# Kernel optimization log

Hardware: AMD Instinct MI355X
Metric: run time of the kernel (lower is better)

Reference implementation:

```python
import jax, jax.numpy as jnp
import numpy as np

N, E, F_NODE, F_EDGE, H, C = 25000, 50000, 7, 2, 4, 512
HC = H * C  # 2048


def setup_inputs() -> dict:
    key = jax.random.key(0)
    ks = jax.random.split(key, 20)
    p = lambda k, shp: (jax.random.normal(k, shp, dtype=jnp.float32) * 0.02)
    return {
        "x": jax.random.normal(ks[0], (N, F_NODE), dtype=jnp.float32),
        "edge_attr": jax.random.normal(ks[1], (E, F_EDGE), dtype=jnp.float32),
        "edge_index": jax.random.randint(ks[2], (2, E), 0, N, dtype=jnp.int64),
        "W_node": p(ks[3], (F_NODE, C)), "b_node": jnp.zeros((C,), jnp.float32),
        "W_edge": p(ks[4], (F_EDGE, C)), "b_edge": jnp.zeros((C,), jnp.float32),
        "W_l": p(ks[5], (C, HC)), "b_l": jnp.zeros((HC,), jnp.float32),
        "W_r": p(ks[6], (C, HC)), "b_r": jnp.zeros((HC,), jnp.float32),
        "W_le": p(ks[7], (C, HC)),  # lin_edge has no bias in PyG GATv2Conv
        "att": p(ks[8], (H, C)),
        "conv_bias": jnp.zeros((HC,), jnp.float32),
        "W_d1": p(ks[9], (HC, C)), "b_d1": jnp.zeros((C,), jnp.float32),
        "W_d2": p(ks[10], (C, 6)), "b_d2": jnp.zeros((6,), jnp.float32),
    }


def reference(x, edge_attr, edge_index, W_node, b_node, W_edge, b_edge,
              W_l, b_l, W_r, b_r, W_le, att, conv_bias, W_d1, b_d1, W_d2, b_d2):
    n = x.shape[0]
    src, dst = edge_index[0], edge_index[1]
    # encoders
    h = jax.nn.relu(x @ W_node + b_node)                  # [N, C]
    ea = jax.nn.relu(edge_attr @ W_edge + b_edge)         # [E, C]
    # GATv2Conv (heads=4, concat, edge_dim, add_self_loops=False)
    xl = (h @ W_l + b_l).reshape(n, H, C)                 # source transform
    xr = (h @ W_r + b_r).reshape(n, H, C)                 # target transform
    ee = (ea @ W_le).reshape(-1, H, C)                    # [E, H, C]
    m = xl[src] + xr[dst] + ee                            # [E, H, C]
    s = jax.nn.leaky_relu(m, negative_slope=0.2)
    logits = jnp.einsum('ehc,hc->eh', s, att)             # [E, H]
    # segment softmax over destination nodes
    mx = jax.ops.segment_max(logits, dst, num_segments=n)
    ex = jnp.exp(logits - mx[dst])
    den = jax.ops.segment_sum(ex, dst, num_segments=n)
    alpha = ex / (den[dst] + 1e-16)                       # [E, H]
    out = jax.ops.segment_sum(alpha[..., None] * xl[src], dst, num_segments=n)
    out = out.reshape(n, HC) + conv_bias                  # [N, 2048]
    # decoder + sigmoid (mode != 'train')
    pred = jax.nn.relu(out @ W_d1 + b_d1) @ W_d2 + b_d2   # [N, 6]
    return jax.nn.sigmoid(pred)
```

## Files before the change

### kernel.cpp

```cpp
#include <hip/hip_runtime.h>
#include <hip/hip_bf16.h>

typedef __attribute__((ext_vector_type(8))) short short8;
typedef __attribute__((ext_vector_type(4))) float f32x4;
typedef unsigned int uint32;

#define GLD16(g, l) __builtin_amdgcn_global_load_lds( \
    (const __attribute__((address_space(1))) unsigned int*)(g), \
    (__attribute__((address_space(3))) unsigned int*)(l), 16, 0, 0)

__device__ __forceinline__ float bfu(unsigned short u) {
    union { uint32 v; float f; } x; x.v = ((uint32)u) << 16; return x.f;
}
__device__ __forceinline__ void storev(float* p, float v) { *p = v; }
__device__ __forceinline__ void storev(__hip_bfloat16* p, float v) { *p = __float2bfloat16(v); }

__global__ __launch_bounds__(256) void transpose_bf16(
    const float* __restrict__ W, __hip_bfloat16* __restrict__ WT, int K, int N)
{
    __shared__ float tile[32][33];
    int k0 = blockIdx.x * 32, n0 = blockIdx.y * 32;
    int tx = threadIdx.x & 31, ty = threadIdx.x >> 5;
    #pragma unroll
    for (int i = 0; i < 32; i += 8)
        tile[ty + i][tx] = W[(size_t)(k0 + ty + i) * N + n0 + tx];
    __syncthreads();
    #pragma unroll
    for (int i = 0; i < 32; i += 8)
        WT[(size_t)(n0 + ty + i) * K + k0 + tx] = __float2bfloat16(tile[tx][ty + i]);
}

__global__ __launch_bounds__(256) void cast_bf16(
    const float* __restrict__ W, __hip_bfloat16* __restrict__ O, int total)
{
    int idx = blockIdx.x * 256 + threadIdx.x;
    if (idx < total) O[idx] = __float2bfloat16(W[idx]);
}

__global__ __launch_bounds__(256) void encode_nodes(
    const float* __restrict__ x, const float* __restrict__ Wn,
    const float* __restrict__ bn, __hip_bfloat16* __restrict__ h, int Nn)
{
    int idx = blockIdx.x * 256 + threadIdx.x;
    if (idx >= Nn * 512) return;
    int n = idx >> 9, c = idx & 511;
    float acc = bn[c];
    #pragma unroll
    for (int f = 0; f < 7; ++f) acc += x[n * 7 + f] * Wn[f * 512 + c];
    h[idx] = __float2bfloat16(fmaxf(acc, 0.f));
}

__global__ __launch_bounds__(256) void encode_edges_sorted(
    const float* __restrict__ eat, const int* __restrict__ elist,
    const float* __restrict__ We, const float* __restrict__ be,
    __hip_bfloat16* __restrict__ ea, int E)
{
    int idx = blockIdx.x * 256 + threadIdx.x;
    if (idx >= E * 512) return;
    int p = idx >> 9, c = idx & 511;
    int e = elist[p];
    float v = fmaf(eat[e * 2], We[c], fmaf(eat[e * 2 + 1], We[512 + c], be[c]));
    ea[idx] = __float2bfloat16(fmaxf(v, 0.f));
}

template <typename OutT, bool HAS_BIAS>
__global__ __launch_bounds__(256) void mfma_gemm(
    const __hip_bfloat16* __restrict__ A, int lda, long az,
    const __hip_bfloat16* __restrict__ BT, int ldb, long bz,
    const float* __restrict__ bias, long biasz,
    OutT* __restrict__ C, int ldc, long cz, int M, int K)
{
    __shared__ uint4 As4[1024];
    __shared__ uint4 Bs4[1024];
    A  += (long)blockIdx.z * az;
    BT += (long)blockIdx.z * bz;
    C  += (long)blockIdx.z * cz;
    if (HAS_BIAS) bias += (long)blockIdx.z * biasz;
    const int t = threadIdx.x, lane = t & 63, w = t >> 6;
    const int wr = (w >> 1) * 64, wc = (w & 1) * 64;
    const int col0 = blockIdx.x * 128, row0 = blockIdx.y * 128;
    const int lr = lane & 15, lg = lane >> 4;
    const int srow8 = lane >> 3;
    const int sch   = (lane & 7) ^ srow8;
    const int rx = lr & 7;

    const __hip_bfloat16* ApL = A + (size_t)(row0 + srow8) * lda + sch * 8;
    const __hip_bfloat16* BpL = BT + (size_t)(col0 + srow8) * ldb + sch * 8;

    f32x4 acc[4][4];
    #pragma unroll
    for (int m = 0; m < 4; ++m)
        #pragma unroll
        for (int n = 0; n < 4; ++n) acc[m][n] = 0.f;

    for (int k0 = 0; k0 < K; k0 += 64) {
        #pragma unroll
        for (int j = 0; j < 4; ++j) {
            int rb = (w + 4 * j) * 8;
            GLD16(ApL + (size_t)rb * lda + k0, As4 + (w + 4 * j) * 64);
            GLD16(BpL + (size_t)rb * ldb + k0, Bs4 + (w + 4 * j) * 64);
        }
        __syncthreads();
        #pragma unroll
        for (int kk = 0; kk < 2; ++kk) {
            short8 af[4], bfrag[4];
            #pragma unroll
            for (int m = 0; m < 4; ++m) {
                int row = wr + m * 16 + lr;
                af[m] = *(const short8*)((const char*)As4 + row * 128 + (((kk * 4 + lg) ^ rx) << 4));
            }
            #pragma unroll
            for (int n = 0; n < 4; ++n) {
                int row = wc + n * 16 + lr;
                bfrag[n] = *(const short8*)((const char*)Bs4 + row * 128 + (((kk * 4 + lg) ^ rx) << 4));
            }
            #pragma unroll
            for (int m = 0; m < 4; ++m)
                #pragma unroll
                for (int n = 0; n < 4; ++n)
                    acc[m][n] = __builtin_amdgcn_mfma_f32_16x16x32_bf16(af[m], bfrag[n], acc[m][n], 0, 0, 0);
        }
        __syncthreads();
    }

    #pragma unroll
    for (int m = 0; m < 4; ++m) {
        #pragma unroll
        for (int r = 0; r < 4; ++r) {
            int gr = row0 + wr + m * 16 + lg * 4 + r;
            if (gr >= M) continue;
            #pragma unroll
            for (int n = 0; n < 4; ++n) {
                int gc = col0 + wc + n * 16 + lr;
                float v = acc[m][n][r];
                if (HAS_BIAS) v += bias[gc];
                storev(&C[(size_t)gr * ldc + gc], v);
            }
        }
    }
}

__global__ __launch_bounds__(256) void edge_mfma_logits(
    const __hip_bfloat16* __restrict__ ea,
    const __hip_bfloat16* __restrict__ WleT,
    const __hip_bfloat16* __restrict__ XL,
    const __hip_bfloat16* __restrict__ XR,
    const int* __restrict__ ssrc,
    const int* __restrict__ sdst,
    const float* __restrict__ att,
    float* __restrict__ logits,
    int E)
{
    __shared__ uint4 As4[1024];
    __shared__ uint4 Bs4[1024];
    __shared__ int srcs[128], dsts[128];
    const int t = threadIdx.x, lane = t & 63, w = t >> 6;
    const int wr = (w >> 1) * 64, wc = (w & 1) * 64;
    const int col0 = blockIdx.x * 128, row0 = blockIdx.y * 128;
    const int lr = lane & 15, lg = lane >> 4;
    const int srow8 = lane >> 3;
    const int sch   = (lane & 7) ^ srow8;
    const int rx = lr & 7;

    if (t < 128) {
        int ge = row0 + t;
        bool ok = ge < E;
        srcs[t] = ok ? ssrc[ge] : 0;
        dsts[t] = ok ? sdst[ge] : 0;
    }
    const __hip_bfloat16* ApL = ea + (size_t)(row0 + srow8) * 512 + sch * 8;
    const __hip_bfloat16* BpL = WleT + (size_t)(col0 + srow8) * 512 + sch * 8;
    __syncthreads();

    f32x4 acc[4][4];
    #pragma unroll
    for (int m = 0; m < 4; ++m)
        #pragma unroll
        for (int n = 0; n < 4; ++n) acc[m][n] = 0.f;

    for (int k0 = 0; k0 < 512; k0 += 64) {
        #pragma unroll
        for (int j = 0; j < 4; ++j) {
            int rb = (w + 4 * j) * 8;
            GLD16(ApL + (size_t)rb * 512 + k0, As4 + (w + 4 * j) * 64);
            GLD16(BpL + (size_t)rb * 512 + k0, Bs4 + (w + 4 * j) * 64);
        }
        __syncthreads();
        #pragma unroll
        for (int kk = 0; kk < 2; ++kk) {
            short8 af[4], bfrag[4];
            #pragma unroll
            for (int m = 0; m < 4; ++m) {
                int row = wr + m * 16 + lr;
                af[m] = *(const short8*)((const char*)As4 + row * 128 + (((kk * 4 + lg) ^ rx) << 4));
            }
            #pragma unroll
            for (int n = 0; n < 4; ++n) {
                int row = wc + n * 16 + lr;
                bfrag[n] = *(const short8*)((const char*)Bs4 + row * 128 + (((kk * 4 + lg) ^ rx) << 4));
            }
            #pragma unroll
            for (int m = 0; m < 4; ++m)
                #pragma unroll
                for (int n = 0; n < 4; ++n)
                    acc[m][n] = __builtin_amdgcn_mfma_f32_16x16x32_bf16(af[m], bfrag[n], acc[m][n], 0, 0, 0);
        }
        __syncthreads();
    }

    const int hh = col0 >> 9;
    float attv[4];
    #pragma unroll
    for (int n = 0; n < 4; ++n)
        attv[n] = att[hh * 512 + ((col0 + wc + n * 16 + lr) & 511)];
    float part[4][4];
    #pragma unroll
    for (int m = 0; m < 4; ++m)
        #pragma unroll
        for (int r = 0; r < 4; ++r) part[m][r] = 0.f;

    const int prt = (lane & 3) * 8;
    const int r0e = w * 16 + (lane >> 2);
    const int s0 = srcs[r0e], s1 = srcs[r0e + 64];
    const int d0 = dsts[r0e], d1 = dsts[r0e + 64];

    #pragma unroll
    for (int pair = 0; pair < 2; ++pair) {
        #pragma unroll
        for (int sp = 0; sp < 2; ++sp) {
            int ch = pair + sp * 2;
            int cc = col0 + ch * 32;
            GLD16(XL + (size_t)s0 * 2048 + cc + prt, As4 + sp * 512 + w * 64);
            GLD16(XL + (size_t)s1 * 2048 + cc + prt, As4 + sp * 512 + (w + 4) * 64);
            GLD16(XR + (size_t)d0 * 2048 + cc + prt, Bs4 + sp * 512 + w * 64);
            GLD16(XR + (size_t)d1 * 2048 + cc + prt, Bs4 + sp * 512 + (w + 4) * 64);
        }
        __syncthreads();
        #pragma unroll
        for (int sp = 0; sp < 2; ++sp) {
            int ch = pair + sp * 2;
            const char* AsB = (const char*)(As4 + sp * 512);
            const char* BsB = (const char*)(Bs4 + sp * 512);
            #pragma unroll
            for (int n = 0; n < 4; ++n) {
                if (((wc + n * 16) >> 5) != ch) continue;
                int colin = ((n & 1) << 4) + lr;
                #pragma unroll
                for (int m = 0; m < 4; ++m) {
                    #pragma unroll
                    for (int r = 0; r < 4; ++r) {
                        int row = wr + m * 16 + lg * 4 + r;
                        float xl = bfu(*(const unsigned short*)(AsB + row * 64 + colin * 2));
                        float xr = bfu(*(const unsigned short*)(BsB + row * 64 + colin * 2));
                        float mv = acc[m][n][r] + xl + xr;
                        part[m][r] += attv[n] * ((mv > 0.f) ? mv : 0.2f * mv);
                    }
                }
            }
        }
        __syncthreads();
    }
    #pragma unroll
    for (int m = 0; m < 4; ++m) {
        #pragma unroll
        for (int r = 0; r < 4; ++r) {
            float p = part[m][r];
            p += __shfl_xor(p, 1); p += __shfl_xor(p, 2);
            p += __shfl_xor(p, 4); p += __shfl_xor(p, 8);
            int ge = row0 + wr + m * 16 + lg * 4 + r;
            if (lr == 0 && ge < E) atomicAdd(&logits[ge * 4 + hh], p);
        }
    }
}

__global__ __launch_bounds__(256) void count_dst(
    const int* __restrict__ ei, int* __restrict__ cnt, int E)
{
    int e = blockIdx.x * 256 + threadIdx.x;
    if (e < E) atomicAdd(&cnt[ei[E + e]], 1);
}

__global__ __launch_bounds__(1024) void scan_kernel(
    const int* __restrict__ cnt, int* __restrict__ offs, int N)
{
    __shared__ int wsum[16];
    __shared__ int stot;
    __shared__ int carry_s;
    int t = threadIdx.x, lane = t & 63, w = t >> 6;
    if (t == 0) carry_s = 0;
    __syncthreads();
    for (int base = 0; base < N; base += 1024) {
        int v = (base + t < N) ? cnt[base + t] : 0;
        int x = v;
        #pragma unroll
        for (int off = 1; off < 64; off <<= 1) {
            int y = __shfl_up(x, off);
            if (lane >= off) x += y;
        }
        if (lane == 63) wsum[w] = x;
        __syncthreads();
        if (w == 0 && lane < 16) {
            int v0 = wsum[lane];
            int s = v0;
            #pragma unroll
            for (int off = 1; off < 16; off <<= 1) {
                int y = __shfl_up(s, off);
                if (lane >= off) s += y;
            }
            wsum[lane] = s - v0;
            if (lane == 15) stot = s;
        }
        __syncthreads();
        if (base + t < N) offs[base + t] = carry_s + wsum[w] + x - v;
        __syncthreads();
        if (t == 0) carry_s += stot;
    }
    __syncthreads();
    if (t == 0) offs[N] = carry_s;
}

__global__ __launch_bounds__(256) void fill_elist(
    const int* __restrict__ ei, const int* __restrict__ offs,
    int* __restrict__ cnt2, int* __restrict__ elist,
    int* __restrict__ ssrc, int* __restrict__ sdst, int E)
{
    int e = blockIdx.x * 256 + threadIdx.x;
    if (e >= E) return;
    int d = ei[E + e];
    int p = offs[d] + atomicAdd(&cnt2[d], 1);
    elist[p] = e;
    ssrc[p] = ei[e];
    sdst[p] = d;
}

__global__ __launch_bounds__(256) void bias_init(
    const float* __restrict__ bd1, float* __restrict__ bias2, float* __restrict__ blw)
{
    int j = blockIdx.x * 256 + threadIdx.x;
    if (j < 512) { bias2[j] = bd1[j]; blw[j] = 0.f; }
}
__global__ __launch_bounds__(256) void bias_acc(
    const float* __restrict__ cb, const float* __restrict__ bl,
    const float* __restrict__ Wd1, float* __restrict__ bias2, float* __restrict__ blw)
{
    int g = blockIdx.x * 256 + threadIdx.x;
    int j = g & 511, slice = g >> 9;
    float pa = 0.f, pb = 0.f;
    for (int k = slice * 128; k < slice * 128 + 128; ++k) {
        float wv = Wd1[(size_t)k * 512 + j];
        pa += cb[k] * wv;
        pb += bl[k] * wv;
    }
    atomicAdd(&bias2[j], pa);
    atomicAdd(&blw[j], pb);
}

__global__ __launch_bounds__(256) void gat_out(
    const __hip_bfloat16* __restrict__ Y,
    const int* __restrict__ ssrc, const int* __restrict__ offs,
    const float* __restrict__ logits,
    const float* __restrict__ bias2, const float* __restrict__ blw,
    const float* __restrict__ Wd2,
    const float* __restrict__ bd2,
    float* __restrict__ out, int N)
{
    __shared__ float wds[512 * 6];
    int t = threadIdx.x;
    for (int i = t; i < 512 * 6; i += 256) wds[i] = Wd2[i];
    __syncthreads();
    int w = t >> 6, lane = t & 63;
    int dst = blockIdx.x * 4 + w;
    if (dst >= N) return;
    int s = offs[dst], cntE = offs[dst + 1] - s;

    float den[4] = {0.f, 0.f, 0.f, 0.f};
    for (int i = 0; i < cntE; ++i) {
        #pragma unroll
        for (int h = 0; h < 4; ++h) den[h] += expf(logits[(s + i) * 4 + h]);
    }
    float acc[8] = {0.f, 0.f, 0.f, 0.f, 0.f, 0.f, 0.f, 0.f};
    for (int i = 0; i < cntE; ++i) {
        int p = s + i;
        int src = ssrc[p];
        #pragma unroll
        for (int h = 0; h < 4; ++h) {
            float al = expf(logits[p * 4 + h]) / (den[h] + 1e-16f);
            uint4 q = *(const uint4*)((const unsigned short*)Y
                        + ((size_t)src * 4 + h) * 512 + lane * 8);
            acc[0] += al * bfu((unsigned short)(q.x & 0xffff));
            acc[1] += al * bfu((unsigned short)(q.x >> 16));
            acc[2] += al * bfu((unsigned short)(q.y & 0xffff));
            acc[3] += al * bfu((unsigned short)(q.y >> 16));
            acc[4] += al * bfu((unsigned short)(q.z & 0xffff));
            acc[5] += al * bfu((unsigned short)(q.z >> 16));
            acc[6] += al * bfu((unsigned short)(q.w & 0xffff));
            acc[7] += al * bfu((unsigned short)(q.w >> 16));
        }
    }
    float gate = (cntE > 0) ? 1.f : 0.f;
    float p6[6] = {0.f, 0.f, 0.f, 0.f, 0.f, 0.f};
    #pragma unroll
    for (int j = 0; j < 8; ++j) {
        int c = lane * 8 + j;
        float u = fmaxf(acc[j] + bias2[c] + gate * blw[c], 0.f);
        #pragma unroll
        for (int jj = 0; jj < 6; ++jj) p6[jj] += u * wds[c * 6 + jj];
    }
    #pragma unroll
    for (int off = 32; off; off >>= 1)
        #pragma unroll
        for (int jj = 0; jj < 6; ++jj) p6[jj] += __shfl_down(p6[jj], off);
    if (lane == 0) {
        #pragma unroll
        for (int jj = 0; jj < 6; ++jj)
            out[(size_t)dst * 6 + jj] = 1.f / (1.f + expf(-(p6[jj] + bd2[jj])));
    }
}

extern "C" void kernel_launch(void* const* d_in, const int* in_sizes, int n_in,
                              void* d_out, int out_size, void* d_ws, size_t ws_size,
                              hipStream_t stream)
{
    const float* x         = (const float*)d_in[0];
    const float* edge_attr = (const float*)d_in[1];
    const int*   ei        = (const int*)d_in[2];
    const float* W_node = (const float*)d_in[3],  *b_node = (const float*)d_in[4];
    const float* W_edge = (const float*)d_in[5],  *b_edge = (const float*)d_in[6];
    const float* W_l    = (const float*)d_in[7],  *b_l    = (const float*)d_in[8];
    const float* W_r    = (const float*)d_in[9],  *b_r    = (const float*)d_in[10];
    const float* W_le   = (const float*)d_in[11];
    const float* att    = (const float*)d_in[12];
    const float* conv_bias = (const float*)d_in[13];
    const float* W_d1   = (const float*)d_in[14], *b_d1 = (const float*)d_in[15];
    const float* W_d2   = (const float*)d_in[16], *b_d2 = (const float*)d_in[17];
    float* out = (float*)d_out;

    const int N = in_sizes[0] / 7;
    const int E = in_sizes[1] / 2;
    const int MP = (N + 127) & ~127;
    const int EP = (E + 127) & ~127;

    char* ws = (char*)d_ws;
    const size_t szR0 = (size_t)EP * 512 * 2;
    const size_t szX  = (size_t)MP * 2048 * 2;
    const size_t szW  = (size_t)2048 * 512 * 2;
    const size_t szlg = (size_t)E * 4 * 4;
    const size_t szI  = (((size_t)(N + 1) * 4) + 15) & ~(size_t)15;
    const size_t o_XL = szR0;
    const size_t o_XR = o_XL + szX;
    const size_t o_W  = o_XR + szX;
    const size_t o_lg = o_W + 4 * szW;
    const size_t o_b2 = o_lg + szlg;
    const size_t o_blw = o_b2 + 2048;
    const size_t o_bc = o_blw + 2048;
    const size_t o_cnt = o_bc + 4096 * 4;
    const size_t o_cnt2 = o_cnt + szI;
    const size_t o_off = o_cnt2 + szI;
    const size_t o_el = o_off + szI;
    const size_t o_ss = o_el + (size_t)E * 4;
    const size_t o_sd = o_ss + (size_t)E * 4;
    const size_t need = o_sd + (size_t)E * 4;
    if (ws_size < need) return;

    __hip_bfloat16* h   = (__hip_bfloat16*)ws;
    __hip_bfloat16* ea  = (__hip_bfloat16*)ws;
    __hip_bfloat16* XL  = (__hip_bfloat16*)(ws + o_XL);
    __hip_bfloat16* XR  = (__hip_bfloat16*)(ws + o_XR);
    __hip_bfloat16* Y   = XR;
    __hip_bfloat16* WlT = (__hip_bfloat16*)(ws + o_W);
    __hip_bfloat16* WrT = WlT + szW / 2;
    __hip_bfloat16* WleT= WrT + szW / 2;
    __hip_bfloat16* WcombT = WleT + szW / 2;
    __hip_bfloat16* Wd1T_t = (__hip_bfloat16*)(ws + o_XL);
    __hip_bfloat16* Wlbf_t = (__hip_bfloat16*)(ws + o_XL + szW);
    float* logits = (float*)(ws + o_lg);
    float* bias2  = (float*)(ws + o_b2);
    float* blw    = (float*)(ws + o_blw);
    float* bcat   = (float*)(ws + o_bc);
    int* cnt   = (int*)(ws + o_cnt);
    int* cnt2  = (int*)(ws + o_cnt2);
    int* offs  = (int*)(ws + o_off);
    int* elist = (int*)(ws + o_el);
    int* ssrc  = (int*)(ws + o_ss);
    int* sdst  = (int*)(ws + o_sd);

    hipMemsetAsync(logits, 0, szlg, stream);
    hipMemsetAsync(cnt, 0, szI, stream);
    hipMemsetAsync(cnt2, 0, szI, stream);
    hipMemcpyAsync(bcat, b_l, 2048 * 4, hipMemcpyDeviceToDevice, stream);
    hipMemcpyAsync(bcat + 2048, b_r, 2048 * 4, hipMemcpyDeviceToDevice, stream);

    dim3 gT(512 / 32, 2048 / 32);
    transpose_bf16<<<gT, 256, 0, stream>>>(W_l,  WlT, 512, 2048);
    transpose_bf16<<<gT, 256, 0, stream>>>(W_r,  WrT, 512, 2048);
    transpose_bf16<<<gT, 256, 0, stream>>>(W_le, WleT, 512, 2048);
    dim3 gT2(2048 / 32, 512 / 32);
    transpose_bf16<<<gT2, 256, 0, stream>>>(W_d1, Wd1T_t, 2048, 512);
    cast_bf16<<<(512 * 2048 + 255) / 256, 256, 0, stream>>>(W_l, Wlbf_t, 512 * 2048);

    dim3 gWc(512 / 128, 512 / 128, 4);
    mfma_gemm<__hip_bfloat16, false><<<gWc, 256, 0, stream>>>(
        Wd1T_t, 2048, 512, Wlbf_t, 2048, 512, nullptr, 0,
        WcombT, 512, (long)512 * 512, 512, 512);

    bias_init<<<2, 256, 0, stream>>>(b_d1, bias2, blw);
    bias_acc<<<32, 256, 0, stream>>>(conv_bias, b_l, W_d1, bias2, blw);

    count_dst<<<(E + 255) / 256, 256, 0, stream>>>(ei, cnt, E);
    scan_kernel<<<1, 1024, 0, stream>>>(cnt, offs, N);
    fill_elist<<<(E + 255) / 256, 256, 0, stream>>>(ei, offs, cnt2, elist, ssrc, sdst, E);

    encode_nodes<<<(N * 512 + 255) / 256, 256, 0, stream>>>(x, W_node, b_node, h, N);

    const int MB = MP / 128;
    dim3 gNode(2048 / 128, MB, 2);
    mfma_gemm<__hip_bfloat16, true><<<gNode, 256, 0, stream>>>(
        h, 512, 0, WlT, 512, (long)2048 * 512, bcat, 2048,
        XL, 2048, (long)MP * 2048, N, 512);

    encode_edges_sorted<<<(E * 512 + 255) / 256, 256, 0, stream>>>(
        edge_attr, elist, W_edge, b_edge, ea, E);

    dim3 gE(16, EP / 128);
    edge_mfma_logits<<<gE, 256, 0, stream>>>(ea, WleT, XL, XR, ssrc, sdst, att, logits, E);

    encode_nodes<<<(N * 512 + 255) / 256, 256, 0, stream>>>(x, W_node, b_node, h, N);

    dim3 gY(2048 / 128, MB);
    mfma_gemm<__hip_bfloat16, false><<<gY, 256, 0, stream>>>(
        h, 512, 0, WcombT, 512, 0, nullptr, 0, Y, 2048, 0, N, 512);

    gat_out<<<(N + 3) / 4, 256, 0, stream>>>(Y, ssrc, offs, logits,
                                             bias2, blw, W_d2, b_d2, out, N);
}
```

Measured before the change: 710.9 us.

## Aggregate encoded node features before the combined projection GEMM

The order of neighbor aggregation and the fused W_l·W_d1 projection is swapped. Each edge now gathers a 512-wide bf16 node feature row and accumulates it per head into a 2048-wide buffer G. A new GEMM with K=2048 then maps G to the 512-wide decoder hidden layer, fusing the bias, the zero-in-degree gate and ReLU. A separate decoder kernel applies the final 6-output layer and sigmoid. This cuts random gather traffic per edge by four times, but adds full writes and reads of the G and Z intermediates and one more kernel launch.

```diff
diff --git a/kernel.cpp b/kernel.cpp
--- a/kernel.cpp
+++ b/kernel.cpp
@@ -135,6 +135,79 @@
                 float v = acc[m][n][r];
                 if (HAS_BIAS) v += bias[gc];
                 storev(&C[(size_t)gr * ldc + gc], v);
+            }
+        }
+    }
+}
+
+__global__ __launch_bounds__(256) void z_gemm(
+    const __hip_bfloat16* __restrict__ A,
+    const __hip_bfloat16* __restrict__ BT,
+    const float* __restrict__ bias2, const float* __restrict__ blw,
+    const int* __restrict__ offs,
+    float* __restrict__ C, int M)
+{
+    __shared__ uint4 As4[1024];
+    __shared__ uint4 Bs4[1024];
+    const int t = threadIdx.x, lane = t & 63, w = t >> 6;
+    const int wr = (w >> 1) * 64, wc = (w & 1) * 64;
+    const int col0 = blockIdx.x * 128, row0 = blockIdx.y * 128;
+    const int lr = lane & 15, lg = lane >> 4;
+    const int srow8 = lane >> 3;
+    const int sch   = (lane & 7) ^ srow8;
+    const int rx = lr & 7;
+
+    const __hip_bfloat16* ApL = A + (size_t)(row0 + srow8) * 2048 + sch * 8;
+    const __hip_bfloat16* BpL = BT + (size_t)(col0 + srow8) * 2048 + sch * 8;
+
+    f32x4 acc[4][4];
+    #pragma unroll
+    for (int m = 0; m < 4; ++m)
+        #pragma unroll
+        for (int n = 0; n < 4; ++n) acc[m][n] = 0.f;
+
+    for (int k0 = 0; k0 < 2048; k0 += 64) {
+        #pragma unroll
+        for (int j = 0; j < 4; ++j) {
+            int rb = (w + 4 * j) * 8;
+            GLD16(ApL + (size_t)rb * 2048 + k0, As4 + (w + 4 * j) * 64);
+            GLD16(BpL + (size_t)rb * 2048 + k0, Bs4 + (w + 4 * j) * 64);
+        }
+        __syncthreads();
+        #pragma unroll
+        for (int kk = 0; kk < 2; ++kk) {
+            short8 af[4], bfrag[4];
+            #pragma unroll
+            for (int m = 0; m < 4; ++m) {
+                int row = wr + m * 16 + lr;
+                af[m] = *(const short8*)((const char*)As4 + row * 128 + (((kk * 4 + lg) ^ rx) << 4));
+            }
+            #pragma unroll
+            for (int n = 0; n < 4; ++n) {
+                int row = wc + n * 16 + lr;
+                bfrag[n] = *(const short8*)((const char*)Bs4 + row * 128 + (((kk * 4 + lg) ^ rx) << 4));
+            }
+            #pragma unroll
+            for (int m = 0; m < 4; ++m)
+                #pragma unroll
+                for (int n = 0; n < 4; ++n)
+                    acc[m][n] = __builtin_amdgcn_mfma_f32_16x16x32_bf16(af[m], bfrag[n], acc[m][n], 0, 0, 0);
+        }
+        __syncthreads();
+    }
+
+    #pragma unroll
+    for (int m = 0; m < 4; ++m) {
+        #pragma unroll
+        for (int r = 0; r < 4; ++r) {
+            int gr = row0 + wr + m * 16 + lg * 4 + r;
+            if (gr >= M) continue;
+            float gate = (offs[gr + 1] > offs[gr]) ? 1.f : 0.f;
+            #pragma unroll
+            for (int n = 0; n < 4; ++n) {
+                int gc = col0 + wc + n * 16 + lr;
+                float v = acc[m][n][r] + bias2[gc] + gate * blw[gc];
+                C[(size_t)gr * 512 + gc] = fmaxf(v, 0.f);
             }
         }
     }
@@ -355,65 +428,78 @@
     atomicAdd(&blw[j], pb);
 }
 
-__global__ __launch_bounds__(256) void gat_out(
-    const __hip_bfloat16* __restrict__ Y,
+__global__ __launch_bounds__(256) void gat_agg(
+    const __hip_bfloat16* __restrict__ hfeat,
     const int* __restrict__ ssrc, const int* __restrict__ offs,
     const float* __restrict__ logits,
-    const float* __restrict__ bias2, const float* __restrict__ blw,
-    const float* __restrict__ Wd2,
-    const float* __restrict__ bd2,
-    float* __restrict__ out, int N)
+    __hip_bfloat16* __restrict__ G,
+    int N)
+{
+    int t = threadIdx.x;
+    int w = t >> 6, lane = t & 63;
+    int dst = blockIdx.x * 4 + w;
+    if (dst >= N) return;
+    int s = offs[dst], cntE = offs[dst + 1] - s;
+
+    float den[4] = {0.f, 0.f, 0.f, 0.f};
+    for (int i = 0; i < cntE; ++i) {
+        #pragma unroll
+        for (int hh = 0; hh < 4; ++hh) den[hh] += expf(logits[(s + i) * 4 + hh]);
+    }
+    float acc[4][8] = {};
+    for (int i = 0; i < cntE; ++i) {
+        int p = s + i;
+        int src = ssrc[p];
+        uint4 q = *(const uint4*)((const unsigned short*)hfeat + (size_t)src * 512 + lane * 8);
+        float hv[8];
+        hv[0] = bfu((unsigned short)(q.x & 0xffff)); hv[1] = bfu((unsigned short)(q.x >> 16));
+        hv[2] = bfu((unsigned short)(q.y & 0xffff)); hv[3] = bfu((unsigned short)(q.y >> 16));
+        hv[4] = bfu((unsigned short)(q.z & 0xffff)); hv[5] = bfu((unsigned short)(q.z >> 16));
+        hv[6] = bfu((unsigned short)(q.w & 0xffff)); hv[7] = bfu((unsigned short)(q.w >> 16));
+        #pragma unroll
+        for (int hh = 0; hh < 4; ++hh) {
+            float al = expf(logits[p * 4 + hh]) / (den[hh] + 1e-16f);
+            #pragma unroll
+            for (int j = 0; j < 8; ++j) acc[hh][j] += al * hv[j];
+        }
+    }
+    #pragma unroll
+    for (int hh = 0; hh < 4; ++hh) {
+        alignas(16) __hip_bfloat16 tmp[8];
+        #pragma unroll
+        for (int j = 0; j < 8; ++j) tmp[j] = __float2bfloat16(acc[hh][j]);
+        *(uint4*)((unsigned short*)G + ((size_t)dst * 4 + hh) * 512 + lane * 8) = *(const uint4*)tmp;
+    }
+}
+
+__global__ __launch_bounds__(256) void decoder(
+    const float* __restrict__ Z, const float* __restrict__ Wd2,
+    const float* __restrict__ bd2, float* __restrict__ out, int M)
 {
     __shared__ float wds[512 * 6];
     int t = threadIdx.x;
     for (int i = t; i < 512 * 6; i += 256) wds[i] = Wd2[i];
     __syncthreads();
-    int w = t >> 6, lane = t & 63;
-    int dst = blockIdx.x * 4 + w;
-    if (dst >= N) return;
-    int s = offs[dst], cntE = offs[dst + 1] - s;
-
-    float den[4] = {0.f, 0.f, 0.f, 0.f};
-    for (int i = 0; i < cntE; ++i) {
-        #pragma unroll
-        for (int h = 0; h < 4; ++h) den[h] += expf(logits[(s + i) * 4 + h]);
-    }
-    float acc[8] = {0.f, 0.f, 0.f, 0.f, 0.f, 0.f, 0.f, 0.f};
-    for (int i = 0; i < cntE; ++i) {
-        int p = s + i;
-        int src = ssrc[p];
-        #pragma unroll
-        for (int h = 0; h < 4; ++h) {
-            float al = expf(logits[p * 4 + h]) / (den[h] + 1e-16f);
-            uint4 q = *(const uint4*)((const unsigned short*)Y
-                        + ((size_t)src * 4 + h) * 512 + lane * 8);
-            acc[0] += al * bfu((unsigned short)(q.x & 0xffff));
-            acc[1] += al * bfu((unsigned short)(q.x >> 16));
-            acc[2] += al * bfu((unsigned short)(q.y & 0xffff));
-            acc[3] += al * bfu((unsigned short)(q.y >> 16));
-            acc[4] += al * bfu((unsigned short)(q.z & 0xffff));
-            acc[5] += al * bfu((unsigned short)(q.z >> 16));
-            acc[6] += al * bfu((unsigned short)(q.w & 0xffff));
-            acc[7] += al * bfu((unsigned short)(q.w >> 16));
-        }
-    }
-    float gate = (cntE > 0) ? 1.f : 0.f;
-    float p6[6] = {0.f, 0.f, 0.f, 0.f, 0.f, 0.f};
-    #pragma unroll
-    for (int j = 0; j < 8; ++j) {
-        int c = lane * 8 + j;
-        float u = fmaxf(acc[j] + bias2[c] + gate * blw[c], 0.f);
-        #pragma unroll
-        for (int jj = 0; jj < 6; ++jj) p6[jj] += u * wds[c * 6 + jj];
+    int node = (blockIdx.x * 256 + t) >> 6;
+    int lane = t & 63;
+    if (node >= M) return;
+    const float* zr = Z + (size_t)node * 512;
+    float p[6] = {0.f, 0.f, 0.f, 0.f, 0.f, 0.f};
+    #pragma unroll
+    for (int k = 0; k < 8; ++k) {
+        int c = lane + k * 64;
+        float a = zr[c];
+        #pragma unroll
+        for (int j = 0; j < 6; ++j) p[j] += a * wds[c * 6 + j];
     }
     #pragma unroll
     for (int off = 32; off; off >>= 1)
         #pragma unroll
-        for (int jj = 0; jj < 6; ++jj) p6[jj] += __shfl_down(p6[jj], off);
+        for (int j = 0; j < 6; ++j) p[j] += __shfl_down(p[j], off);
     if (lane == 0) {
         #pragma unroll
-        for (int jj = 0; jj < 6; ++jj)
-            out[(size_t)dst * 6 + jj] = 1.f / (1.f + expf(-(p6[jj] + bd2[jj])));
+        for (int j = 0; j < 6; ++j)
+            out[(size_t)node * 6 + j] = 1.f / (1.f + expf(-(p[j] + bd2[j])));
     }
 }
 
@@ -464,13 +550,14 @@
 
     __hip_bfloat16* h   = (__hip_bfloat16*)ws;
     __hip_bfloat16* ea  = (__hip_bfloat16*)ws;
+    float*          Z   = (float*)ws;
     __hip_bfloat16* XL  = (__hip_bfloat16*)(ws + o_XL);
     __hip_bfloat16* XR  = (__hip_bfloat16*)(ws + o_XR);
-    __hip_bfloat16* Y   = XR;
+    __hip_bfloat16* G   = XR;
     __hip_bfloat16* WlT = (__hip_bfloat16*)(ws + o_W);
     __hip_bfloat16* WrT = WlT + szW / 2;
     __hip_bfloat16* WleT= WrT + szW / 2;
-    __hip_bfloat16* WcombT = WleT + szW / 2;
+    __hip_bfloat16* WcombT2 = WleT + szW / 2;
     __hip_bfloat16* Wd1T_t = (__hip_bfloat16*)(ws + o_XL);
     __hip_bfloat16* Wlbf_t = (__hip_bfloat16*)(ws + o_XL + szW);
     float* logits = (float*)(ws + o_lg);
@@ -501,7 +588,7 @@
     dim3 gWc(512 / 128, 512 / 128, 4);
     mfma_gemm<__hip_bfloat16, false><<<gWc, 256, 0, stream>>>(
         Wd1T_t, 2048, 512, Wlbf_t, 2048, 512, nullptr, 0,
-        WcombT, 512, (long)512 * 512, 512, 512);
+        WcombT2, 2048, 512, 512, 512);
 
     bias_init<<<2, 256, 0, stream>>>(b_d1, bias2, blw);
     bias_acc<<<32, 256, 0, stream>>>(conv_bias, b_l, W_d1, bias2, blw);
@@ -525,11 +612,10 @@
     edge_mfma_logits<<<gE, 256, 0, stream>>>(ea, WleT, XL, XR, ssrc, sdst, att, logits, E);
 
     encode_nodes<<<(N * 512 + 255) / 256, 256, 0, stream>>>(x, W_node, b_node, h, N);
-
-    dim3 gY(2048 / 128, MB);
-    mfma_gemm<__hip_bfloat16, false><<<gY, 256, 0, stream>>>(
-        h, 512, 0, WcombT, 512, 0, nullptr, 0, Y, 2048, 0, N, 512);
-
-    gat_out<<<(N + 3) / 4, 256, 0, stream>>>(Y, ssrc, offs, logits,
-                                             bias2, blw, W_d2, b_d2, out, N);
-}
+    gat_agg<<<(N + 3) / 4, 256, 0, stream>>>(h, ssrc, offs, logits, G, N);
+
+    dim3 gZ(512 / 128, MB);
+    z_gemm<<<gZ, 256, 0, stream>>>(G, WcombT2, bias2, blw, offs, Z, N);
+
+    decoder<<<(N * 64 + 255) / 256, 256, 0, stream>>>(Z, W_d2, b_d2, out, N);
+}
```

After: 749.9 us. 1.05x slower.

## Fold node projections into edge GEMM via concatenated K dimension

Applied to the files above, without the earlier changes.

The XL/XR node GEMMs are no longer materialised and then gathered per edge. The edge logits kernel now runs one GEMM with K=1536 over the concatenation [edge features, h[src], h[dst]] against a stacked transposed weight [W_le; W_l; W_r], with the biases b_l + b_r added in the epilogue. This removes the large XL/XR write and gather traffic, the separate bias-concat copies, and a duplicate node-encoding launch. In exchange the edge GEMM does roughly three times the MFMA work, since node projections are recomputed once per edge instead of once per node.

```diff
diff --git a/kernel.cpp b/kernel.cpp
--- a/kernel.cpp
+++ b/kernel.cpp
@@ -16,7 +16,8 @@
 __device__ __forceinline__ void storev(__hip_bfloat16* p, float v) { *p = __float2bfloat16(v); }
 
 __global__ __launch_bounds__(256) void transpose_bf16(
-    const float* __restrict__ W, __hip_bfloat16* __restrict__ WT, int K, int N)
+    const float* __restrict__ W, __hip_bfloat16* __restrict__ WT,
+    int K, int N, int outld)
 {
     __shared__ float tile[32][33];
     int k0 = blockIdx.x * 32, n0 = blockIdx.y * 32;
@@ -27,7 +28,7 @@
     __syncthreads();
     #pragma unroll
     for (int i = 0; i < 32; i += 8)
-        WT[(size_t)(n0 + ty + i) * K + k0 + tx] = __float2bfloat16(tile[tx][ty + i]);
+        WT[(size_t)(n0 + ty + i) * outld + k0 + tx] = __float2bfloat16(tile[tx][ty + i]);
 }
 
 __global__ __launch_bounds__(256) void cast_bf16(
@@ -140,14 +141,13 @@
     }
 }
 
-__global__ __launch_bounds__(256) void edge_mfma_logits(
+__global__ __launch_bounds__(256) void logits_mfma(
     const __hip_bfloat16* __restrict__ ea,
-    const __hip_bfloat16* __restrict__ WleT,
-    const __hip_bfloat16* __restrict__ XL,
-    const __hip_bfloat16* __restrict__ XR,
-    const int* __restrict__ ssrc,
-    const int* __restrict__ sdst,
+    const __hip_bfloat16* __restrict__ hfeat,
+    const __hip_bfloat16* __restrict__ WbigT,
+    const int* __restrict__ ssrc, const int* __restrict__ sdst,
     const float* __restrict__ att,
+    const float* __restrict__ bl, const float* __restrict__ br,
     float* __restrict__ logits,
     int E)
 {
@@ -168,22 +168,34 @@
         srcs[t] = ok ? ssrc[ge] : 0;
         dsts[t] = ok ? sdst[ge] : 0;
     }
-    const __hip_bfloat16* ApL = ea + (size_t)(row0 + srow8) * 512 + sch * 8;
-    const __hip_bfloat16* BpL = WleT + (size_t)(col0 + srow8) * 512 + sch * 8;
     __syncthreads();
 
+    const __hip_bfloat16* pe[4];
+    const __hip_bfloat16* ps[4];
+    const __hip_bfloat16* pd[4];
+    #pragma unroll
+    for (int j = 0; j < 4; ++j) {
+        int row = (w + 4 * j) * 8 + srow8;
+        pe[j] = ea + (size_t)(row0 + row) * 512 + sch * 8;
+        ps[j] = hfeat + (size_t)srcs[row] * 512 + sch * 8;
+        pd[j] = hfeat + (size_t)dsts[row] * 512 + sch * 8;
+    }
+    const __hip_bfloat16* BpL = WbigT + (size_t)(col0 + srow8) * 1536 + sch * 8;
+
     f32x4 acc[4][4];
     #pragma unroll
     for (int m = 0; m < 4; ++m)
         #pragma unroll
         for (int n = 0; n < 4; ++n) acc[m][n] = 0.f;
 
-    for (int k0 = 0; k0 < 512; k0 += 64) {
+    for (int k0 = 0; k0 < 1536; k0 += 64) {
+        const int ksub = k0 & 511;
         #pragma unroll
         for (int j = 0; j < 4; ++j) {
-            int rb = (w + 4 * j) * 8;
-            GLD16(ApL + (size_t)rb * 512 + k0, As4 + (w + 4 * j) * 64);
-            GLD16(BpL + (size_t)rb * 512 + k0, Bs4 + (w + 4 * j) * 64);
+            const __hip_bfloat16* base =
+                (k0 < 512) ? pe[j] : (k0 < 1024) ? ps[j] : pd[j];
+            GLD16(base + ksub, As4 + (w + 4 * j) * 64);
+            GLD16(BpL + (size_t)((w + 4 * j) * 8) * 1536 + k0, Bs4 + (w + 4 * j) * 64);
         }
         __syncthreads();
         #pragma unroll
@@ -209,66 +221,27 @@
     }
 
     const int hh = col0 >> 9;
-    float attv[4];
-    #pragma unroll
-    for (int n = 0; n < 4; ++n)
-        attv[n] = att[hh * 512 + ((col0 + wc + n * 16 + lr) & 511)];
-    float part[4][4];
-    #pragma unroll
-    for (int m = 0; m < 4; ++m)
-        #pragma unroll
-        for (int r = 0; r < 4; ++r) part[m][r] = 0.f;
-
-    const int prt = (lane & 3) * 8;
-    const int r0e = w * 16 + (lane >> 2);
-    const int s0 = srcs[r0e], s1 = srcs[r0e + 64];
-    const int d0 = dsts[r0e], d1 = dsts[r0e + 64];
-
-    #pragma unroll
-    for (int pair = 0; pair < 2; ++pair) {
-        #pragma unroll
-        for (int sp = 0; sp < 2; ++sp) {
-            int ch = pair + sp * 2;
-            int cc = col0 + ch * 32;
-            GLD16(XL + (size_t)s0 * 2048 + cc + prt, As4 + sp * 512 + w * 64);
-            GLD16(XL + (size_t)s1 * 2048 + cc + prt, As4 + sp * 512 + (w + 4) * 64);
-            GLD16(XR + (size_t)d0 * 2048 + cc + prt, Bs4 + sp * 512 + w * 64);
-            GLD16(XR + (size_t)d1 * 2048 + cc + prt, Bs4 + sp * 512 + (w + 4) * 64);
-        }
-        __syncthreads();
-        #pragma unroll
-        for (int sp = 0; sp < 2; ++sp) {
-            int ch = pair + sp * 2;
-            const char* AsB = (const char*)(As4 + sp * 512);
-            const char* BsB = (const char*)(Bs4 + sp * 512);
+    float attv[4], bcv[4];
+    #pragma unroll
+    for (int n = 0; n < 4; ++n) {
+        int gc = col0 + wc + n * 16 + lr;
+        attv[n] = att[hh * 512 + (gc & 511)];
+        bcv[n] = bl[gc] + br[gc];
+    }
+    #pragma unroll
+    for (int m = 0; m < 4; ++m) {
+        #pragma unroll
+        for (int r = 0; r < 4; ++r) {
+            float part = 0.f;
             #pragma unroll
             for (int n = 0; n < 4; ++n) {
-                if (((wc + n * 16) >> 5) != ch) continue;
-                int colin = ((n & 1) << 4) + lr;
-                #pragma unroll
-                for (int m = 0; m < 4; ++m) {
-                    #pragma unroll
-                    for (int r = 0; r < 4; ++r) {
-                        int row = wr + m * 16 + lg * 4 + r;
-                        float xl = bfu(*(const unsigned short*)(AsB + row * 64 + colin * 2));
-                        float xr = bfu(*(const unsigned short*)(BsB + row * 64 + colin * 2));
-                        float mv = acc[m][n][r] + xl + xr;
-                        part[m][r] += attv[n] * ((mv > 0.f) ? mv : 0.2f * mv);
-                    }
-                }
-            }
-        }
-        __syncthreads();
-    }
-    #pragma unroll
-    for (int m = 0; m < 4; ++m) {
-        #pragma unroll
-        for (int r = 0; r < 4; ++r) {
-            float p = part[m][r];
-            p += __shfl_xor(p, 1); p += __shfl_xor(p, 2);
-            p += __shfl_xor(p, 4); p += __shfl_xor(p, 8);
+                float mv = acc[m][n][r] + bcv[n];
+                part += attv[n] * ((mv > 0.f) ? mv : 0.2f * mv);
+            }
+            part += __shfl_xor(part, 1); part += __shfl_xor(part, 2);
+            part += __shfl_xor(part, 4); part += __shfl_xor(part, 8);
             int ge = row0 + wr + m * 16 + lg * 4 + r;
-            if (lr == 0 && ge < E) atomicAdd(&logits[ge * 4 + hh], p);
+            if (lr == 0 && ge < E) atomicAdd(&logits[ge * 4 + hh], part);
         }
     }
 }
@@ -441,42 +414,42 @@
     const int EP = (E + 127) & ~127;
 
     char* ws = (char*)d_ws;
-    const size_t szR0 = (size_t)EP * 512 * 2;
-    const size_t szX  = (size_t)MP * 2048 * 2;
+    const size_t szH  = (size_t)MP * 512 * 2;
+    const size_t szEA = (size_t)EP * 512 * 2;
+    const size_t szY  = (size_t)MP * 2048 * 2;
+    const size_t szWb = (size_t)2048 * 1536 * 2;
     const size_t szW  = (size_t)2048 * 512 * 2;
     const size_t szlg = (size_t)E * 4 * 4;
     const size_t szI  = (((size_t)(N + 1) * 4) + 15) & ~(size_t)15;
-    const size_t o_XL = szR0;
-    const size_t o_XR = o_XL + szX;
-    const size_t o_W  = o_XR + szX;
-    const size_t o_lg = o_W + 4 * szW;
-    const size_t o_b2 = o_lg + szlg;
+    const size_t o_h   = 0;
+    const size_t o_ea  = o_h + szH;
+    const size_t o_Y   = o_ea + szEA;
+    const size_t o_Wb  = o_Y + szY;
+    const size_t o_Wc  = o_Wb + szWb;
+    const size_t o_Wt1 = o_Wc + szW;
+    const size_t o_Wt2 = o_Wt1 + szW;
+    const size_t o_lg  = o_Wt2 + szW;
+    const size_t o_b2  = o_lg + szlg;
     const size_t o_blw = o_b2 + 2048;
-    const size_t o_bc = o_blw + 2048;
-    const size_t o_cnt = o_bc + 4096 * 4;
+    const size_t o_cnt = o_blw + 2048;
     const size_t o_cnt2 = o_cnt + szI;
     const size_t o_off = o_cnt2 + szI;
-    const size_t o_el = o_off + szI;
-    const size_t o_ss = o_el + (size_t)E * 4;
-    const size_t o_sd = o_ss + (size_t)E * 4;
-    const size_t need = o_sd + (size_t)E * 4;
+    const size_t o_el  = o_off + szI;
+    const size_t o_ss  = o_el + (size_t)E * 4;
+    const size_t o_sd  = o_ss + (size_t)E * 4;
+    const size_t need  = o_sd + (size_t)E * 4;
     if (ws_size < need) return;
 
-    __hip_bfloat16* h   = (__hip_bfloat16*)ws;
-    __hip_bfloat16* ea  = (__hip_bfloat16*)ws;
-    __hip_bfloat16* XL  = (__hip_bfloat16*)(ws + o_XL);
-    __hip_bfloat16* XR  = (__hip_bfloat16*)(ws + o_XR);
-    __hip_bfloat16* Y   = XR;
-    __hip_bfloat16* WlT = (__hip_bfloat16*)(ws + o_W);
-    __hip_bfloat16* WrT = WlT + szW / 2;
-    __hip_bfloat16* WleT= WrT + szW / 2;
-    __hip_bfloat16* WcombT = WleT + szW / 2;
-    __hip_bfloat16* Wd1T_t = (__hip_bfloat16*)(ws + o_XL);
-    __hip_bfloat16* Wlbf_t = (__hip_bfloat16*)(ws + o_XL + szW);
+    __hip_bfloat16* h    = (__hip_bfloat16*)(ws + o_h);
+    __hip_bfloat16* ea   = (__hip_bfloat16*)(ws + o_ea);
+    __hip_bfloat16* Y    = (__hip_bfloat16*)(ws + o_Y);
+    __hip_bfloat16* WbigT= (__hip_bfloat16*)(ws + o_Wb);
+    __hip_bfloat16* WcombT = (__hip_bfloat16*)(ws + o_Wc);
+    __hip_bfloat16* Wd1T_t = (__hip_bfloat16*)(ws + o_Wt1);
+    __hip_bfloat16* Wlbf_t = (__hip_bfloat16*)(ws + o_Wt2);
     float* logits = (float*)(ws + o_lg);
     float* bias2  = (float*)(ws + o_b2);
     float* blw    = (float*)(ws + o_blw);
-    float* bcat   = (float*)(ws + o_bc);
     int* cnt   = (int*)(ws + o_cnt);
     int* cnt2  = (int*)(ws + o_cnt2);
     int* offs  = (int*)(ws + o_off);
@@ -487,15 +460,13 @@
     hipMemsetAsync(logits, 0, szlg, stream);
     hipMemsetAsync(cnt, 0, szI, stream);
     hipMemsetAsync(cnt2, 0, szI, stream);
-    hipMemcpyAsync(bcat, b_l, 2048 * 4, hipMemcpyDeviceToDevice, stream);
-    hipMemcpyAsync(bcat + 2048, b_r, 2048 * 4, hipMemcpyDeviceToDevice, stream);
 
     dim3 gT(512 / 32, 2048 / 32);
-    transpose_bf16<<<gT, 256, 0, stream>>>(W_l,  WlT, 512, 2048);
-    transpose_bf16<<<gT, 256, 0, stream>>>(W_r,  WrT, 512, 2048);
-    transpose_bf16<<<gT, 256, 0, stream>>>(W_le, WleT, 512, 2048);
+    transpose_bf16<<<gT, 256, 0, stream>>>(W_le, WbigT,        512, 2048, 1536);
+    transpose_bf16<<<gT, 256, 0, stream>>>(W_l,  WbigT + 512,  512, 2048, 1536);
+    transpose_bf16<<<gT, 256, 0, stream>>>(W_r,  WbigT + 1024, 512, 2048, 1536);
     dim3 gT2(2048 / 32, 512 / 32);
-    transpose_bf16<<<gT2, 256, 0, stream>>>(W_d1, Wd1T_t, 2048, 512);
+    transpose_bf16<<<gT2, 256, 0, stream>>>(W_d1, Wd1T_t, 2048, 512, 2048);
     cast_bf16<<<(512 * 2048 + 255) / 256, 256, 0, stream>>>(W_l, Wlbf_t, 512 * 2048);
 
     dim3 gWc(512 / 128, 512 / 128, 4);
@@ -511,22 +482,15 @@
     fill_elist<<<(E + 255) / 256, 256, 0, stream>>>(ei, offs, cnt2, elist, ssrc, sdst, E);
 
     encode_nodes<<<(N * 512 + 255) / 256, 256, 0, stream>>>(x, W_node, b_node, h, N);
-
-    const int MB = MP / 128;
-    dim3 gNode(2048 / 128, MB, 2);
-    mfma_gemm<__hip_bfloat16, true><<<gNode, 256, 0, stream>>>(
-        h, 512, 0, WlT, 512, (long)2048 * 512, bcat, 2048,
-        XL, 2048, (long)MP * 2048, N, 512);
-
     encode_edges_sorted<<<(E * 512 + 255) / 256, 256, 0, stream>>>(
         edge_attr, elist, W_edge, b_edge, ea, E);
 
-    dim3 gE(16, EP / 128);
-    edge_mfma_logits<<<gE, 256, 0, stream>>>(ea, WleT, XL, XR, ssrc, sdst, att, logits, E);
-
-    encode_nodes<<<(N * 512 + 255) / 256, 256, 0, stream>>>(x, W_node, b_node, h, N);
-
-    dim3 gY(2048 / 128, MB);
+    dim3 gL(16, EP / 128);
+    logits_mfma<<<gL, 256, 0, stream>>>(ea, h, WbigT, ssrc, sdst, att,
+                                        b_l, b_r, logits, E);
+
+    const int MB = MP / 128;
+    dim3 gY(16, MB);
     mfma_gemm<__hip_bfloat16, false><<<gY, 256, 0, stream>>>(
         h, 512, 0, WcombT, 512, 0, nullptr, 0, Y, 2048, 0, N, 512);
 
```

After: 734.1 us. +3.3%, slower.

## Merge weight transposes, parallelize CSR scan, fold bias init into accumulation

Applied to the files above, without the earlier changes.

Replaces the three per-weight transpose launches with a single launch that uses blockIdx.z to pick the matrix. Replaces the single-block serial prefix scan over node counts with a three-phase multi-block scan (block sums, a scan of those sums, then a final pass), and writes offs[N]=E directly. Drops the bias_init kernel by memsetting bias2/blw and seeding b_d1 inside bias_acc. These changes cut launch count and the serial scan latency, at the cost of two extra small launches for the scan and a scan_tops that only handles up to 128 blocks.

```diff
diff --git a/kernel.cpp b/kernel.cpp
--- a/kernel.cpp
+++ b/kernel.cpp
@@ -14,6 +14,24 @@
 }
 __device__ __forceinline__ void storev(float* p, float v) { *p = v; }
 __device__ __forceinline__ void storev(__hip_bfloat16* p, float v) { *p = __float2bfloat16(v); }
+
+__global__ __launch_bounds__(256) void transpose3_bf16(
+    const float* __restrict__ W0, const float* __restrict__ W1,
+    const float* __restrict__ W2, __hip_bfloat16* __restrict__ WT)
+{
+    __shared__ float tile[32][33];
+    const float* W = (blockIdx.z == 0) ? W0 : (blockIdx.z == 1) ? W1 : W2;
+    __hip_bfloat16* O = WT + (size_t)blockIdx.z * 2048 * 512;
+    int k0 = blockIdx.x * 32, n0 = blockIdx.y * 32;
+    int tx = threadIdx.x & 31, ty = threadIdx.x >> 5;
+    #pragma unroll
+    for (int i = 0; i < 32; i += 8)
+        tile[ty + i][tx] = W[(size_t)(k0 + ty + i) * 2048 + n0 + tx];
+    __syncthreads();
+    #pragma unroll
+    for (int i = 0; i < 32; i += 8)
+        O[(size_t)(n0 + ty + i) * 512 + k0 + tx] = __float2bfloat16(tile[tx][ty + i]);
+}
 
 __global__ __launch_bounds__(256) void transpose_bf16(
     const float* __restrict__ W, __hip_bfloat16* __restrict__ WT, int K, int N)
@@ -280,43 +298,57 @@
     if (e < E) atomicAdd(&cnt[ei[E + e]], 1);
 }
 
-__global__ __launch_bounds__(1024) void scan_kernel(
-    const int* __restrict__ cnt, int* __restrict__ offs, int N)
-{
-    __shared__ int wsum[16];
-    __shared__ int stot;
-    __shared__ int carry_s;
+__global__ __launch_bounds__(256) void scan_sums(
+    const int* __restrict__ cnt, int* __restrict__ bsum, int N)
+{
+    __shared__ int wsums[4];
+    int t = threadIdx.x;
+    int idx = blockIdx.x * 256 + t;
+    int v = (idx < N) ? cnt[idx] : 0;
+    #pragma unroll
+    for (int o = 32; o; o >>= 1) v += __shfl_down(v, o);
+    if ((t & 63) == 0) wsums[t >> 6] = v;
+    __syncthreads();
+    if (t == 0) bsum[blockIdx.x] = wsums[0] + wsums[1] + wsums[2] + wsums[3];
+}
+
+__global__ __launch_bounds__(128) void scan_tops(int* __restrict__ bsum, int nb)
+{
+    __shared__ int s0;
     int t = threadIdx.x, lane = t & 63, w = t >> 6;
-    if (t == 0) carry_s = 0;
-    __syncthreads();
-    for (int base = 0; base < N; base += 1024) {
-        int v = (base + t < N) ? cnt[base + t] : 0;
-        int x = v;
-        #pragma unroll
-        for (int off = 1; off < 64; off <<= 1) {
-            int y = __shfl_up(x, off);
-            if (lane >= off) x += y;
-        }
-        if (lane == 63) wsum[w] = x;
-        __syncthreads();
-        if (w == 0 && lane < 16) {
-            int v0 = wsum[lane];
-            int s = v0;
-            #pragma unroll
-            for (int off = 1; off < 16; off <<= 1) {
-                int y = __shfl_up(s, off);
-                if (lane >= off) s += y;
-            }
-            wsum[lane] = s - v0;
-            if (lane == 15) stot = s;
-        }
-        __syncthreads();
-        if (base + t < N) offs[base + t] = carry_s + wsum[w] + x - v;
-        __syncthreads();
-        if (t == 0) carry_s += stot;
-    }
-    __syncthreads();
-    if (t == 0) offs[N] = carry_s;
+    int v = (t < nb) ? bsum[t] : 0;
+    int x = v;
+    #pragma unroll
+    for (int o = 1; o < 64; o <<= 1) {
+        int y = __shfl_up(x, o);
+        if (lane >= o) x += y;
+    }
+    if (w == 0 && lane == 63) s0 = x;
+    __syncthreads();
+    int ex = x - v + (w ? s0 : 0);
+    if (t < nb) bsum[t] = ex;
+}
+
+__global__ __launch_bounds__(256) void scan_final(
+    const int* __restrict__ cnt, const int* __restrict__ boff,
+    int* __restrict__ offs, int N, int E)
+{
+    __shared__ int wsums[4];
+    int t = threadIdx.x, lane = t & 63, w = t >> 6;
+    int idx = blockIdx.x * 256 + t;
+    int v = (idx < N) ? cnt[idx] : 0;
+    int x = v;
+    #pragma unroll
+    for (int o = 1; o < 64; o <<= 1) {
+        int y = __shfl_up(x, o);
+        if (lane >= o) x += y;
+    }
+    if (lane == 63) wsums[w] = x;
+    __syncthreads();
+    int add = boff[blockIdx.x];
+    for (int i = 0; i < w; ++i) add += wsums[i];
+    if (idx < N) offs[idx] = add + x - v;
+    if (blockIdx.x == 0 && t == 0) offs[N] = E;
 }
 
 __global__ __launch_bounds__(256) void fill_elist(
@@ -333,19 +365,14 @@
     sdst[p] = d;
 }
 
-__global__ __launch_bounds__(256) void bias_init(
-    const float* __restrict__ bd1, float* __restrict__ bias2, float* __restrict__ blw)
-{
-    int j = blockIdx.x * 256 + threadIdx.x;
-    if (j < 512) { bias2[j] = bd1[j]; blw[j] = 0.f; }
-}
 __global__ __launch_bounds__(256) void bias_acc(
-    const float* __restrict__ cb, const float* __restrict__ bl,
-    const float* __restrict__ Wd1, float* __restrict__ bias2, float* __restrict__ blw)
+    const float* __restrict__ bd1, const float* __restrict__ cb,
+    const float* __restrict__ bl, const float* __restrict__ Wd1,
+    float* __restrict__ bias2, float* __restrict__ blw)
 {
     int g = blockIdx.x * 256 + threadIdx.x;
     int j = g & 511, slice = g >> 9;
-    float pa = 0.f, pb = 0.f;
+    float pa = (slice == 0) ? bd1[j] : 0.f, pb = 0.f;
     for (int k = slice * 128; k < slice * 128 + 128; ++k) {
         float wv = Wd1[(size_t)k * 512 + j];
         pa += cb[k] * wv;
@@ -439,6 +466,7 @@
     const int E = in_sizes[1] / 2;
     const int MP = (N + 127) & ~127;
     const int EP = (E + 127) & ~127;
+    const int NB = (N + 255) / 256;
 
     char* ws = (char*)d_ws;
     const size_t szR0 = (size_t)EP * 512 * 2;
@@ -459,7 +487,8 @@
     const size_t o_el = o_off + szI;
     const size_t o_ss = o_el + (size_t)E * 4;
     const size_t o_sd = o_ss + (size_t)E * 4;
-    const size_t need = o_sd + (size_t)E * 4;
+    const size_t o_bs = o_sd + (size_t)E * 4;
+    const size_t need = o_bs + 512;
     if (ws_size < need) return;
 
     __hip_bfloat16* h   = (__hip_bfloat16*)ws;
@@ -468,9 +497,8 @@
     __hip_bfloat16* XR  = (__hip_bfloat16*)(ws + o_XR);
     __hip_bfloat16* Y   = XR;
     __hip_bfloat16* WlT = (__hip_bfloat16*)(ws + o_W);
-    __hip_bfloat16* WrT = WlT + szW / 2;
-    __hip_bfloat16* WleT= WrT + szW / 2;
-    __hip_bfloat16* WcombT = WleT + szW / 2;
+    __hip_bfloat16* WleT= WlT + szW;
+    __hip_bfloat16* WcombT = (__hip_bfloat16*)(ws + o_W) + 3 * (szW / 2);
     __hip_bfloat16* Wd1T_t = (__hip_bfloat16*)(ws + o_XL);
     __hip_bfloat16* Wlbf_t = (__hip_bfloat16*)(ws + o_XL + szW);
     float* logits = (float*)(ws + o_lg);
@@ -483,17 +511,17 @@
     int* elist = (int*)(ws + o_el);
     int* ssrc  = (int*)(ws + o_ss);
     int* sdst  = (int*)(ws + o_sd);
+    int* bsum  = (int*)(ws + o_bs);
 
     hipMemsetAsync(logits, 0, szlg, stream);
     hipMemsetAsync(cnt, 0, szI, stream);
     hipMemsetAsync(cnt2, 0, szI, stream);
+    hipMemsetAsync(bias2, 0, 4096, stream);
     hipMemcpyAsync(bcat, b_l, 2048 * 4, hipMemcpyDeviceToDevice, stream);
     hipMemcpyAsync(bcat + 2048, b_r, 2048 * 4, hipMemcpyDeviceToDevice, stream);
 
-    dim3 gT(512 / 32, 2048 / 32);
-    transpose_bf16<<<gT, 256, 0, stream>>>(W_l,  WlT, 512, 2048);
-    transpose_bf16<<<gT, 256, 0, stream>>>(W_r,  WrT, 512, 2048);
-    transpose_bf16<<<gT, 256, 0, stream>>>(W_le, WleT, 512, 2048);
+    dim3 gT3(512 / 32, 2048 / 32, 3);
+    transpose3_bf16<<<gT3, 256, 0, stream>>>(W_l, W_r, W_le, WlT);
     dim3 gT2(2048 / 32, 512 / 32);
     transpose_bf16<<<gT2, 256, 0, stream>>>(W_d1, Wd1T_t, 2048, 512);
     cast_bf16<<<(512 * 2048 + 255) / 256, 256, 0, stream>>>(W_l, Wlbf_t, 512 * 2048);
@@ -503,11 +531,12 @@
         Wd1T_t, 2048, 512, Wlbf_t, 2048, 512, nullptr, 0,
         WcombT, 512, (long)512 * 512, 512, 512);
 
-    bias_init<<<2, 256, 0, stream>>>(b_d1, bias2, blw);
-    bias_acc<<<32, 256, 0, stream>>>(conv_bias, b_l, W_d1, bias2, blw);
+    bias_acc<<<32, 256, 0, stream>>>(b_d1, conv_bias, b_l, W_d1, bias2, blw);
 
     count_dst<<<(E + 255) / 256, 256, 0, stream>>>(ei, cnt, E);
-    scan_kernel<<<1, 1024, 0, stream>>>(cnt, offs, N);
+    scan_sums<<<NB, 256, 0, stream>>>(cnt, bsum, N);
+    scan_tops<<<1, 128, 0, stream>>>(bsum, NB);
+    scan_final<<<NB, 256, 0, stream>>>(cnt, bsum, offs, N, E);
     fill_elist<<<(E + 255) / 256, 256, 0, stream>>>(ei, offs, cnt2, elist, ssrc, sdst, E);
 
     encode_nodes<<<(N * 512 + 255) / 256, 256, 0, stream>>>(x, W_node, b_node, h, N);
```

New measurement: 686.6 us. 1.04x faster.
